# Kernel optimization log

Measured on AMD Instinct MI355X. Metric: run time of the kernel, lower is better.

Reference implementation:

```python
import jax, jax.numpy as jnp
import numpy as np

DIM = 1024
HEADS = 16
HEAD_DIM = DIM // HEADS
SCALE = HEAD_DIM ** -0.5


def setup_inputs() -> dict:
    key = jax.random.key(0)
    k1, k2, k3 = jax.random.split(key, 3)
    x = jax.random.normal(k1, (4, 2048, DIM), dtype=jnp.float32)
    Wqkv = jax.random.normal(k2, (DIM, 3 * DIM), dtype=jnp.float32) * (DIM ** -0.5)
    Wout = jax.random.normal(k3, (DIM, DIM), dtype=jnp.float32) * (DIM ** -0.5)
    bout = jnp.zeros((DIM,), dtype=jnp.float32)
    return {"x": x, "Wqkv": Wqkv, "Wout": Wout, "bout": bout}


def reference(x, Wqkv, Wout, bout):
    b, n, _ = x.shape
    qkv = x @ Wqkv  # [b, n, 3*dim]
    q, k, v = jnp.split(qkv, 3, axis=-1)
    # [b, n, dim] -> [b, h, n, d]
    def split_heads(t):
        return t.reshape(b, n, HEADS, HEAD_DIM).transpose(0, 2, 1, 3)
    q, k, v = split_heads(q), split_heads(k), split_heads(v)
    dots = jnp.einsum('bhid,bhjd->bhij', q, k) * SCALE
    attn = jax.nn.softmax(dots, axis=-1)
    out = jnp.einsum('bhij,bhjd->bhid', attn, v)
    out = out.transpose(0, 2, 1, 3).reshape(b, n, DIM)
    return out @ Wout + bout  # dropout is identity in eval mode
```

## Files before the change

kernel.cpp:

```cpp
#include <hip/hip_runtime.h>
#include <hip/hip_bf16.h>

#define BATCH 4
#define SEQ   2048
#define DIM   1024
#define HEADS 16
#define HD    64
#define ROWS  (BATCH * SEQ)
#define QKV_N (3 * DIM)
#define ATT_C 0.18033688011f

typedef unsigned short u16;
typedef _Float16 half8 __attribute__((ext_vector_type(8)));
typedef _Float16 half4v __attribute__((ext_vector_type(4)));
typedef float f32x4 __attribute__((ext_vector_type(4)));

__device__ __forceinline__ void gload_lds16(const u16* g, u16* l) {
  typedef const __attribute__((address_space(1))) unsigned int* gp_t;
  typedef __attribute__((address_space(3))) unsigned int* lp_t;
  __builtin_amdgcn_global_load_lds((gp_t)(const void*)g, (lp_t)(void*)l, 16, 0, 0);
}

__global__ __launch_bounds__(256) void conv_x(const float* __restrict__ x,
                                              u16* __restrict__ xh) {
  int i = blockIdx.x * 256 + threadIdx.x;
  float4 v = ((const float4*)x)[i];
  half4v h = {(_Float16)v.x, (_Float16)v.y, (_Float16)v.z, (_Float16)v.w};
  *(half4v*)&xh[(size_t)i * 4] = h;
}

__global__ __launch_bounds__(256) void conv_w(const float* __restrict__ W,
                                              u16* __restrict__ Wt,
                                              int K, int N) {
  __shared__ float T[64][65];
  const int tid = threadIdx.x;
  const int k0 = blockIdx.y * 64, n0 = blockIdx.x * 64;
#pragma unroll
  for (int j = 0; j < 4; ++j) {
    int k = j * 16 + (tid >> 4), n4 = (tid & 15) * 4;
    float4 v = *(const float4*)(W + (size_t)(k0 + k) * N + n0 + n4);
    T[k][n4 + 0] = v.x; T[k][n4 + 1] = v.y; T[k][n4 + 2] = v.z; T[k][n4 + 3] = v.w;
  }
  __syncthreads();
#pragma unroll
  for (int j = 0; j < 4; ++j) {
    int n = j * 16 + (tid >> 4), k4 = (tid & 15) * 4;
    half4v w = {(_Float16)T[k4 + 0][n], (_Float16)T[k4 + 1][n],
                (_Float16)T[k4 + 2][n], (_Float16)T[k4 + 3][n]};
    *(half4v*)&Wt[(size_t)(n0 + n) * K + k0 + k4] = w;
  }
}

template <int MODE>
__global__ __launch_bounds__(256) void gemm_bt(
    const u16* __restrict__ A, const u16* __restrict__ Bt,
    const float* __restrict__ bias, void* __restrict__ Cv,
    u16* __restrict__ Qg, u16* __restrict__ Kg, u16* __restrict__ VtG,
    int M, int N, int K) {
  __shared__ u16 As[128 * 32];
  __shared__ u16 Bs[128 * 32];

  const int tid = threadIdx.x;
  const int wave = tid >> 6, lane = tid & 63;
  const int q4 = lane >> 4, c = lane & 15;
  const int wm = wave >> 1, wn = wave & 1;
  const int row0 = blockIdx.y * 128, col0 = blockIdx.x * 128;
  const int rr = lane >> 2, seg = lane & 3;

  f32x4 acc[4][4];
#pragma unroll
  for (int mi = 0; mi < 4; ++mi)
#pragma unroll
    for (int ni = 0; ni < 4; ++ni) acc[mi][ni] = (f32x4){0.f, 0.f, 0.f, 0.f};

  for (int k0 = 0; k0 < K; k0 += 32) {
#pragma unroll
    for (int i = 0; i < 2; ++i) {
      int chunk = wave * 2 + i;
      gload_lds16(A + (size_t)(row0 + chunk * 16 + rr) * K + k0 + seg * 8,
                  &As[chunk * 512]);
      gload_lds16(Bt + (size_t)(col0 + chunk * 16 + rr) * K + k0 + seg * 8,
                  &Bs[chunk * 512]);
    }
    __syncthreads();

    half8 af[4], bf[4];
#pragma unroll
    for (int mi = 0; mi < 4; ++mi)
      af[mi] = *(const half8*)&As[(wm * 64 + mi * 16 + c) * 32 + q4 * 8];
#pragma unroll
    for (int ni = 0; ni < 4; ++ni)
      bf[ni] = *(const half8*)&Bs[(wn * 64 + ni * 16 + c) * 32 + q4 * 8];
#pragma unroll
    for (int mi = 0; mi < 4; ++mi)
#pragma unroll
      for (int ni = 0; ni < 4; ++ni)
        acc[mi][ni] = __builtin_amdgcn_mfma_f32_16x16x32_f16(
            af[mi], bf[ni], acc[mi][ni], 0, 0, 0);
    __syncthreads();
  }

#pragma unroll
  for (int mi = 0; mi < 4; ++mi)
#pragma unroll
    for (int ni = 0; ni < 4; ++ni) {
      int colg = col0 + wn * 64 + ni * 16 + c;
      if (MODE == 0) {
        float bv = bias[colg];
#pragma unroll
        for (int r = 0; r < 4; ++r) {
          int rowg = row0 + wm * 64 + mi * 16 + q4 * 4 + r;
          ((float*)Cv)[(size_t)rowg * N + colg] = acc[mi][ni][r] + bv;
        }
      } else {
        int rowg0 = row0 + wm * 64 + mi * 16 + q4 * 4;
        int b  = rowg0 >> 11;
        int which = colg >> 10;
        int rem = colg & 1023;
        int hh = rem >> 6, d = rem & 63;
        size_t bh = (size_t)(b * HEADS + hh);
        if (which == 2) {
          int i0 = rowg0 & 2047;
          half4v pv = {(_Float16)acc[mi][ni][0], (_Float16)acc[mi][ni][1],
                       (_Float16)acc[mi][ni][2], (_Float16)acc[mi][ni][3]};
          *(half4v*)&VtG[(bh * HD + d) * SEQ + i0] = pv;
        } else {
          u16* dst = (which == 0) ? Qg : Kg;
#pragma unroll
          for (int r = 0; r < 4; ++r) {
            int i = (rowg0 + r) & 2047;
            ((_Float16*)dst)[(bh * SEQ + i) * HD + d] = (_Float16)acc[mi][ni][r];
          }
        }
      }
    }
}

__global__ __launch_bounds__(256) void attn_mfma(
    const u16* __restrict__ Qg, const u16* __restrict__ Kg,
    const u16* __restrict__ VtG, u16* __restrict__ ctx) {
  const int qt = blockIdx.x;
  const int h  = blockIdx.y;
  const int b  = blockIdx.z;

  __shared__ u16 Qs[2][64 * 32];
  __shared__ u16 Ks[2][64 * 32];
  __shared__ u16 Vt[2][64 * 32];
  __shared__ u16 Ps[64 * 72];
  __shared__ float lred[4][64];
  __shared__ float lfull[64];

  const int tid  = threadIdx.x;
  const int wave = tid >> 6;
  const int lane = tid & 63;
  const int q4   = lane >> 4;
  const int c    = lane & 15;
  const int rr   = lane >> 2, seg = lane & 3;

  const size_t bh = (size_t)(b * HEADS + h);
  const int qrow0 = qt * 64;

#pragma unroll
  for (int half = 0; half < 2; ++half)
    gload_lds16(Qg + (bh * SEQ + qrow0 + wave * 16 + rr) * HD + half * 32 + seg * 8,
                &Qs[half][wave * 16 * 32]);
  __syncthreads();

  half8 qf[4][2];
#pragma unroll
  for (int nt = 0; nt < 4; ++nt)
#pragma unroll
    for (int half = 0; half < 2; ++half)
      qf[nt][half] = *(const half8*)&Qs[half][(nt * 16 + c) * 32 + q4 * 8];

  f32x4 o_acc[4];
#pragma unroll
  for (int dt = 0; dt < 4; ++dt) o_acc[dt] = (f32x4){0.f, 0.f, 0.f, 0.f};
  float lp[4] = {0.f, 0.f, 0.f, 0.f};

  for (int j0 = 0; j0 < SEQ; j0 += 64) {
    __syncthreads();
#pragma unroll
    for (int half = 0; half < 2; ++half) {
      gload_lds16(Kg + (bh * SEQ + j0 + wave * 16 + rr) * HD + half * 32 + seg * 8,
                  &Ks[half][wave * 16 * 32]);
      gload_lds16(VtG + (bh * HD + wave * 16 + rr) * SEQ + j0 + half * 32 + seg * 8,
                  &Vt[half][wave * 16 * 32]);
    }
    __syncthreads();

    half8 af0 = *(const half8*)&Ks[0][(wave * 16 + c) * 32 + q4 * 8];
    half8 af1 = *(const half8*)&Ks[1][(wave * 16 + c) * 32 + q4 * 8];
    f32x4 st[4];
#pragma unroll
    for (int nt = 0; nt < 4; ++nt) {
      st[nt] = (f32x4){0.f, 0.f, 0.f, 0.f};
      st[nt] = __builtin_amdgcn_mfma_f32_16x16x32_f16(af0, qf[nt][0], st[nt], 0, 0, 0);
      st[nt] = __builtin_amdgcn_mfma_f32_16x16x32_f16(af1, qf[nt][1], st[nt], 0, 0, 0);
    }

#pragma unroll
    for (int nt = 0; nt < 4; ++nt) {
      float p0 = __builtin_amdgcn_exp2f(st[nt][0] * ATT_C);
      float p1 = __builtin_amdgcn_exp2f(st[nt][1] * ATT_C);
      float p2 = __builtin_amdgcn_exp2f(st[nt][2] * ATT_C);
      float p3 = __builtin_amdgcn_exp2f(st[nt][3] * ATT_C);
      lp[nt] += (p0 + p1) + (p2 + p3);
      half4v w = {(_Float16)p0, (_Float16)p1, (_Float16)p2, (_Float16)p3};
      *(half4v*)&Ps[(nt * 16 + c) * 72 + wave * 16 + q4 * 4] = w;
    }
    __syncthreads();

    half8 pa0 = *(const half8*)&Ps[(wave * 16 + c) * 72 + q4 * 8];
    half8 pa1 = *(const half8*)&Ps[(wave * 16 + c) * 72 + 32 + q4 * 8];
#pragma unroll
    for (int dt = 0; dt < 4; ++dt) {
      half8 v0 = *(const half8*)&Vt[0][(dt * 16 + c) * 32 + q4 * 8];
      half8 v1 = *(const half8*)&Vt[1][(dt * 16 + c) * 32 + q4 * 8];
      o_acc[dt] = __builtin_amdgcn_mfma_f32_16x16x32_f16(pa0, v0, o_acc[dt], 0, 0, 0);
      o_acc[dt] = __builtin_amdgcn_mfma_f32_16x16x32_f16(pa1, v1, o_acc[dt], 0, 0, 0);
    }
  }

#pragma unroll
  for (int nt = 0; nt < 4; ++nt) {
    lp[nt] += __shfl_xor(lp[nt], 16);
    lp[nt] += __shfl_xor(lp[nt], 32);
  }
  if (q4 == 0)
#pragma unroll
    for (int nt = 0; nt < 4; ++nt) lred[wave][nt * 16 + c] = lp[nt];
  __syncthreads();
  if (wave == 0 && q4 == 0)
#pragma unroll
    for (int nt = 0; nt < 4; ++nt) {
      int i = nt * 16 + c;
      lfull[i] = lred[0][i] + lred[1][i] + lred[2][i] + lred[3][i];
    }
  __syncthreads();

#pragma unroll
  for (int r = 0; r < 4; ++r) {
    float inv = 1.0f / lfull[wave * 16 + q4 * 4 + r];
    size_t row = (size_t)b * SEQ + qrow0 + wave * 16 + q4 * 4 + r;
#pragma unroll
    for (int dt = 0; dt < 4; ++dt)
      ((_Float16*)ctx)[row * DIM + h * HD + dt * 16 + c] =
          (_Float16)(o_acc[dt][r] * inv);
  }
}

extern "C" void kernel_launch(void* const* d_in, const int* in_sizes, int n_in,
                              void* d_out, int out_size, void* d_ws, size_t ws_size,
                              hipStream_t stream) {
  const float* x    = (const float*)d_in[0];
  const float* Wqkv = (const float*)d_in[1];
  const float* Wout = (const float*)d_in[2];
  const float* bout = (const float*)d_in[3];
  float* out = (float*)d_out;

  u16* xh   = (u16*)d_ws;
  u16* Wqt  = xh  + (size_t)ROWS * DIM;
  u16* Wot  = Wqt + (size_t)QKV_N * DIM;
  u16* Qg   = Wot + (size_t)DIM * DIM;
  u16* Kg   = Qg  + (size_t)BATCH * HEADS * SEQ * HD;
  u16* VtG  = Kg  + (size_t)BATCH * HEADS * SEQ * HD;
  u16* ctxh = VtG + (size_t)BATCH * HEADS * HD * SEQ;

  conv_x<<<ROWS * DIM / 4 / 256, 256, 0, stream>>>(x, xh);
  conv_w<<<dim3(QKV_N / 64, DIM / 64), 256, 0, stream>>>(Wqkv, Wqt, DIM, QKV_N);
  conv_w<<<dim3(DIM / 64, DIM / 64), 256, 0, stream>>>(Wout, Wot, DIM, DIM);

  gemm_bt<1><<<dim3(QKV_N / 128, ROWS / 128), 256, 0, stream>>>(
      xh, Wqt, nullptr, nullptr, Qg, Kg, VtG, ROWS, QKV_N, DIM);

  attn_mfma<<<dim3(SEQ / 64, HEADS, BATCH), 256, 0, stream>>>(Qg, Kg, VtG, ctxh);

  gemm_bt<0><<<dim3(DIM / 128, ROWS / 128), 256, 0, stream>>>(
      ctxh, Wot, bout, out, nullptr, nullptr, nullptr, ROWS, DIM, DIM);
}
```

Baseline: 308.7 us.

## Double attention query tile to 128 rows, swizzle LDS, fold softmax scale into Q

Each attention block now processes 128 query rows instead of 64, so every K/V tile loaded into shared memory feeds twice as many MFMAs. LDS chunk positions are XOR-swizzled to reduce bank conflicts on the fragment reads. The softmax scale is folded into Q in the QKV GEMM epilogue, removing a multiply per score. The grid is flattened with batch-head as the fastest index and launch bounds are set for 3 blocks per CU. The trade-off is more registers and shared memory per block and half as many blocks in the grid.

Measured after the change: 301.5 us. 1.02x faster.

```diff
diff --git a/kernel.cpp b/kernel.cpp
--- a/kernel.cpp
+++ b/kernel.cpp
@@ -126,29 +126,32 @@
           *(half4v*)&VtG[(bh * HD + d) * SEQ + i0] = pv;
         } else {
           u16* dst = (which == 0) ? Qg : Kg;
+          float sc = (which == 0) ? ATT_C : 1.0f;
 #pragma unroll
           for (int r = 0; r < 4; ++r) {
             int i = (rowg0 + r) & 2047;
-            ((_Float16*)dst)[(bh * SEQ + i) * HD + d] = (_Float16)acc[mi][ni][r];
+            ((_Float16*)dst)[(bh * SEQ + i) * HD + d] =
+                (_Float16)(acc[mi][ni][r] * sc);
           }
         }
       }
     }
 }
 
-__global__ __launch_bounds__(256) void attn_mfma(
+__global__ __launch_bounds__(256, 3) void attn_mfma(
     const u16* __restrict__ Qg, const u16* __restrict__ Kg,
     const u16* __restrict__ VtG, u16* __restrict__ ctx) {
-  const int qt = blockIdx.x;
-  const int h  = blockIdx.y;
-  const int b  = blockIdx.z;
-
-  __shared__ u16 Qs[2][64 * 32];
+  const int L  = blockIdx.x;
+  const int bh = L & 63;
+  const int b  = bh >> 4, h = bh & 15;
+  const int qt = L >> 6;
+
+  __shared__ u16 Qs[2][128 * 32];
   __shared__ u16 Ks[2][64 * 32];
   __shared__ u16 Vt[2][64 * 32];
-  __shared__ u16 Ps[64 * 72];
-  __shared__ float lred[4][64];
-  __shared__ float lfull[64];
+  __shared__ u16 Ps[128 * 72];
+  __shared__ float lred[4][128];
+  __shared__ float lfull[128];
 
   const int tid  = threadIdx.x;
   const int wave = tid >> 6;
@@ -156,98 +159,113 @@
   const int q4   = lane >> 4;
   const int c    = lane & 15;
   const int rr   = lane >> 2, seg = lane & 3;
-
-  const size_t bh = (size_t)(b * HEADS + h);
-  const int qrow0 = qt * 64;
+  const int sseg = seg ^ (rr & 3);
+  const int rsw  = (c & 3);
+
+  const size_t bhb = (size_t)bh;
+  const int qrow0 = qt * 128;
 
 #pragma unroll
   for (int half = 0; half < 2; ++half)
-    gload_lds16(Qg + (bh * SEQ + qrow0 + wave * 16 + rr) * HD + half * 32 + seg * 8,
-                &Qs[half][wave * 16 * 32]);
-  __syncthreads();
-
-  half8 qf[4][2];
-#pragma unroll
-  for (int nt = 0; nt < 4; ++nt)
+#pragma unroll
+    for (int i = 0; i < 2; ++i) {
+      int chunk = wave * 2 + i;
+      gload_lds16(Qg + (bhb * SEQ + qrow0 + chunk * 16 + rr) * HD
+                      + half * 32 + sseg * 8,
+                  &Qs[half][chunk * 16 * 32]);
+    }
+  __syncthreads();
+
+  half8 qf[8][2];
+#pragma unroll
+  for (int nt = 0; nt < 8; ++nt)
 #pragma unroll
     for (int half = 0; half < 2; ++half)
-      qf[nt][half] = *(const half8*)&Qs[half][(nt * 16 + c) * 32 + q4 * 8];
-
-  f32x4 o_acc[4];
-#pragma unroll
-  for (int dt = 0; dt < 4; ++dt) o_acc[dt] = (f32x4){0.f, 0.f, 0.f, 0.f};
-  float lp[4] = {0.f, 0.f, 0.f, 0.f};
+      qf[nt][half] =
+          *(const half8*)&Qs[half][(nt * 16 + c) * 32 + (q4 ^ rsw) * 8];
+
+  f32x4 o_acc[2][4];
+#pragma unroll
+  for (int sub = 0; sub < 2; ++sub)
+#pragma unroll
+    for (int dt = 0; dt < 4; ++dt) o_acc[sub][dt] = (f32x4){0.f, 0.f, 0.f, 0.f};
+  float lp[8] = {0.f, 0.f, 0.f, 0.f, 0.f, 0.f, 0.f, 0.f};
 
   for (int j0 = 0; j0 < SEQ; j0 += 64) {
     __syncthreads();
 #pragma unroll
     for (int half = 0; half < 2; ++half) {
-      gload_lds16(Kg + (bh * SEQ + j0 + wave * 16 + rr) * HD + half * 32 + seg * 8,
+      gload_lds16(Kg + (bhb * SEQ + j0 + wave * 16 + rr) * HD
+                      + half * 32 + sseg * 8,
                   &Ks[half][wave * 16 * 32]);
-      gload_lds16(VtG + (bh * HD + wave * 16 + rr) * SEQ + j0 + half * 32 + seg * 8,
+      gload_lds16(VtG + (bhb * HD + wave * 16 + rr) * SEQ + j0
+                      + half * 32 + sseg * 8,
                   &Vt[half][wave * 16 * 32]);
     }
     __syncthreads();
 
-    half8 af0 = *(const half8*)&Ks[0][(wave * 16 + c) * 32 + q4 * 8];
-    half8 af1 = *(const half8*)&Ks[1][(wave * 16 + c) * 32 + q4 * 8];
-    f32x4 st[4];
-#pragma unroll
-    for (int nt = 0; nt < 4; ++nt) {
-      st[nt] = (f32x4){0.f, 0.f, 0.f, 0.f};
-      st[nt] = __builtin_amdgcn_mfma_f32_16x16x32_f16(af0, qf[nt][0], st[nt], 0, 0, 0);
-      st[nt] = __builtin_amdgcn_mfma_f32_16x16x32_f16(af1, qf[nt][1], st[nt], 0, 0, 0);
-    }
-
-#pragma unroll
-    for (int nt = 0; nt < 4; ++nt) {
-      float p0 = __builtin_amdgcn_exp2f(st[nt][0] * ATT_C);
-      float p1 = __builtin_amdgcn_exp2f(st[nt][1] * ATT_C);
-      float p2 = __builtin_amdgcn_exp2f(st[nt][2] * ATT_C);
-      float p3 = __builtin_amdgcn_exp2f(st[nt][3] * ATT_C);
+    half8 af0 = *(const half8*)&Ks[0][(wave * 16 + c) * 32 + (q4 ^ rsw) * 8];
+    half8 af1 = *(const half8*)&Ks[1][(wave * 16 + c) * 32 + (q4 ^ rsw) * 8];
+#pragma unroll
+    for (int nt = 0; nt < 8; ++nt) {
+      f32x4 st = (f32x4){0.f, 0.f, 0.f, 0.f};
+      st = __builtin_amdgcn_mfma_f32_16x16x32_f16(af0, qf[nt][0], st, 0, 0, 0);
+      st = __builtin_amdgcn_mfma_f32_16x16x32_f16(af1, qf[nt][1], st, 0, 0, 0);
+      float p0 = __builtin_amdgcn_exp2f(st[0]);
+      float p1 = __builtin_amdgcn_exp2f(st[1]);
+      float p2 = __builtin_amdgcn_exp2f(st[2]);
+      float p3 = __builtin_amdgcn_exp2f(st[3]);
       lp[nt] += (p0 + p1) + (p2 + p3);
       half4v w = {(_Float16)p0, (_Float16)p1, (_Float16)p2, (_Float16)p3};
       *(half4v*)&Ps[(nt * 16 + c) * 72 + wave * 16 + q4 * 4] = w;
     }
     __syncthreads();
 
-    half8 pa0 = *(const half8*)&Ps[(wave * 16 + c) * 72 + q4 * 8];
-    half8 pa1 = *(const half8*)&Ps[(wave * 16 + c) * 72 + 32 + q4 * 8];
+    half8 vb0[4], vb1[4];
 #pragma unroll
     for (int dt = 0; dt < 4; ++dt) {
-      half8 v0 = *(const half8*)&Vt[0][(dt * 16 + c) * 32 + q4 * 8];
-      half8 v1 = *(const half8*)&Vt[1][(dt * 16 + c) * 32 + q4 * 8];
-      o_acc[dt] = __builtin_amdgcn_mfma_f32_16x16x32_f16(pa0, v0, o_acc[dt], 0, 0, 0);
-      o_acc[dt] = __builtin_amdgcn_mfma_f32_16x16x32_f16(pa1, v1, o_acc[dt], 0, 0, 0);
-    }
-  }
-
-#pragma unroll
-  for (int nt = 0; nt < 4; ++nt) {
+      vb0[dt] = *(const half8*)&Vt[0][(dt * 16 + c) * 32 + (q4 ^ rsw) * 8];
+      vb1[dt] = *(const half8*)&Vt[1][(dt * 16 + c) * 32 + (q4 ^ rsw) * 8];
+    }
+#pragma unroll
+    for (int sub = 0; sub < 2; ++sub) {
+      half8 pa0 = *(const half8*)&Ps[(wave * 32 + sub * 16 + c) * 72 + q4 * 8];
+      half8 pa1 = *(const half8*)&Ps[(wave * 32 + sub * 16 + c) * 72 + 32 + q4 * 8];
+#pragma unroll
+      for (int dt = 0; dt < 4; ++dt) {
+        o_acc[sub][dt] = __builtin_amdgcn_mfma_f32_16x16x32_f16(
+            pa0, vb0[dt], o_acc[sub][dt], 0, 0, 0);
+        o_acc[sub][dt] = __builtin_amdgcn_mfma_f32_16x16x32_f16(
+            pa1, vb1[dt], o_acc[sub][dt], 0, 0, 0);
+      }
+    }
+  }
+
+#pragma unroll
+  for (int nt = 0; nt < 8; ++nt) {
     lp[nt] += __shfl_xor(lp[nt], 16);
     lp[nt] += __shfl_xor(lp[nt], 32);
   }
   if (q4 == 0)
 #pragma unroll
-    for (int nt = 0; nt < 4; ++nt) lred[wave][nt * 16 + c] = lp[nt];
-  __syncthreads();
-  if (wave == 0 && q4 == 0)
-#pragma unroll
-    for (int nt = 0; nt < 4; ++nt) {
-      int i = nt * 16 + c;
-      lfull[i] = lred[0][i] + lred[1][i] + lred[2][i] + lred[3][i];
-    }
-  __syncthreads();
-
-#pragma unroll
-  for (int r = 0; r < 4; ++r) {
-    float inv = 1.0f / lfull[wave * 16 + q4 * 4 + r];
-    size_t row = (size_t)b * SEQ + qrow0 + wave * 16 + q4 * 4 + r;
-#pragma unroll
-    for (int dt = 0; dt < 4; ++dt)
-      ((_Float16*)ctx)[row * DIM + h * HD + dt * 16 + c] =
-          (_Float16)(o_acc[dt][r] * inv);
-  }
+    for (int nt = 0; nt < 8; ++nt) lred[wave][nt * 16 + c] = lp[nt];
+  __syncthreads();
+  if (tid < 128)
+    lfull[tid] = lred[0][tid] + lred[1][tid] + lred[2][tid] + lred[3][tid];
+  __syncthreads();
+
+#pragma unroll
+  for (int sub = 0; sub < 2; ++sub)
+#pragma unroll
+    for (int r = 0; r < 4; ++r) {
+      int i = wave * 32 + sub * 16 + q4 * 4 + r;
+      float inv = 1.0f / lfull[i];
+      size_t row = (size_t)b * SEQ + qrow0 + i;
+#pragma unroll
+      for (int dt = 0; dt < 4; ++dt)
+        ((_Float16*)ctx)[row * DIM + h * HD + dt * 16 + c] =
+            (_Float16)(o_acc[sub][dt][r] * inv);
+    }
 }
 
 extern "C" void kernel_launch(void* const* d_in, const int* in_sizes, int n_in,
@@ -274,7 +292,7 @@
   gemm_bt<1><<<dim3(QKV_N / 128, ROWS / 128), 256, 0, stream>>>(
       xh, Wqt, nullptr, nullptr, Qg, Kg, VtG, ROWS, QKV_N, DIM);
 
-  attn_mfma<<<dim3(SEQ / 64, HEADS, BATCH), 256, 0, stream>>>(Qg, Kg, VtG, ctxh);
+  attn_mfma<<<dim3(1024), 256, 0, stream>>>(Qg, Kg, VtG, ctxh);
 
   gemm_bt<0><<<dim3(DIM / 128, ROWS / 128), 256, 0, stream>>>(
       ctxh, Wot, bout, out, nullptr, nullptr, nullptr, ROWS, DIM, DIM);
```
